# Kernel tuning notes

Hardware: AMD Instinct MI355X
Metric: run time of the kernel (lower is better)

Reference implementation:

```python
import jax, jax.numpy as jnp
import numpy as np

N0, N1, N2 = 1500, 6000, 4000
F_IN, F_OUT = 32, 32
K00, K0P = 2, 2
K1N, K11, K12, K1P = 2, 2, 2, 2
K2N, K22 = 2, 2


def chebyshev(L, k, x):
    # Chebyshev recursion: T1 = L x, T2 = 2 L T1 - x, T_j = 2 L T_{j-1} - T_{j-2}
    # Returns (n, F, k) stack of T1..Tk (identity term handled by caller).
    t_prev = L @ x
    terms = [t_prev]
    t_pp = x
    for _ in range(k - 1):
        t = 2.0 * (L @ t_prev) - t_pp
        t_pp, t_prev = t_prev, t
        terms.append(t)
    return jnp.stack(terms, axis=2)


def _sym(key, n):
    a = jax.random.normal(key, (n, n), jnp.float32) / jnp.sqrt(jnp.float32(n))
    return 0.5 * (a + a.T)


def setup_inputs():
    key = jax.random.key(0)
    ks = jax.random.split(key, 16)
    x0 = jax.random.normal(ks[0], (N0, F_IN), jnp.float32)
    x1 = jax.random.normal(ks[1], (N1, F_IN), jnp.float32)
    x2 = jax.random.normal(ks[2], (N2, F_IN), jnp.float32)
    B1 = jax.random.normal(ks[3], (N0, N1), jnp.float32) / jnp.sqrt(jnp.float32(N1))
    B2 = jax.random.normal(ks[4], (N1, N2), jnp.float32) / jnp.sqrt(jnp.float32(N2))
    L0 = _sym(ks[5], N0)
    L1l = _sym(ks[6], N1)
    L1u = _sym(ks[7], N1)
    L2 = _sym(ks[8], N2)
    # Degree matrices: diagonal with strictly positive entries (as in real SC data).
    D1 = jnp.diag(jax.random.uniform(ks[9], (N0,), jnp.float32, 0.5, 2.0))
    D2 = jnp.diag(jax.random.uniform(ks[10], (N1,), jnp.float32, 0.5, 2.0))
    D3 = jnp.diag(jax.random.uniform(ks[11], (N2,), jnp.float32, 0.5, 2.0))
    D5 = jnp.diag(jax.random.uniform(ks[12], (N1,), jnp.float32, 0.5, 2.0))
    W0 = jax.random.normal(ks[13], (F_IN, F_OUT, 1 + K00 + 1 + K0P), jnp.float32) * 0.05
    W1 = jax.random.normal(ks[14], (F_IN, F_OUT, 1 + K1N + 1 + K11 + K12 + 1 + K1P), jnp.float32) * 0.05
    W2 = jax.random.normal(ks[15], (F_IN, F_OUT, 1 + K2N + 1 + K22), jnp.float32) * 0.05
    return dict(x0=x0, x1=x1, x2=x2, B1=B1, B2=B2, L0=L0, L1l=L1l, L1u=L1u,
                L2=L2, D1=D1, D2=D2, D3=D3, D5=D5, W0=W0, W1=W1, W2=W2)


def _forward(x0, x1, x2, B1, B2, L0, L1l, L1u, L2, d1_inv, d2, d3, d5_pinv, W0, W1, W2):
    # ---- order 0 ----
    x0p = d1_inv[:, None] * (B1 @ x1)               # inv(D1) @ B1 @ x1
    X0 = jnp.concatenate([x0[:, :, None], chebyshev(L0, K00, x0),
                          x0p[:, :, None], chebyshev(L0, K0P, x0p)], axis=2)
    # ---- order 1 ----
    x1n = d2[:, None] * (B1.T @ (d1_inv[:, None] * x0))  # D2 @ B1.T @ inv(D1) @ x0
    x1p = B2 @ (d3[:, None] * x2)                        # B2 @ D3 @ x2
    X1 = jnp.concatenate([x1n[:, :, None], chebyshev(L1l, K1N, x1n),
                          x1[:, :, None], chebyshev(L1l, K11, x1), chebyshev(L1u, K12, x1),
                          x1p[:, :, None], chebyshev(L1u, K1P, x1p)], axis=2)
    # ---- order 2 ----
    x2n = B2.T @ (d5_pinv[:, None] * x1)                 # B2.T @ pinv(D5) @ x1
    X2 = jnp.concatenate([x2n[:, :, None], chebyshev(L2, K2N, x2n),
                          x2[:, :, None], chebyshev(L2, K22, x2)], axis=2)
    y0 = jax.nn.relu(jnp.einsum('nik,iok->no', X0, W0))
    y1 = jax.nn.relu(jnp.einsum('nik,iok->no', X1, W1))
    y2 = jax.nn.relu(jnp.einsum('nik,iok->no', X2, W2))
    return (y0, y1, y2)


def reference(x0, x1, x2, B1, B2, L0, L1l, L1u, L2, D1, D2, D3, D5, W0, W1, W2):
    # D matrices are diagonal degree matrices; inverse/pinverse of a diagonal
    # matrix is the diagonal of (safe) reciprocals -- identical math to
    # torch.inverse / torch.pinverse on these inputs, without an O(n^3) solve.
    d1_inv = 1.0 / jnp.diag(D1)
    d2 = jnp.diag(D2)
    d3 = jnp.diag(D3)
    d5 = jnp.diag(D5)
    d5_pinv = jnp.where(d5 != 0, 1.0 / d5, 0.0)
    return _forward(x0, x1, x2, B1, B2, L0, L1l, L1u, L2, d1_inv, d2, d3, d5_pinv, W0, W1, W2)
```

## Files before the change

kernel.cpp:

```cpp
#include <hip/hip_runtime.h>
#include <stdint.h>

typedef __attribute__((ext_vector_type(4))) float f32x4;
typedef __attribute__((ext_vector_type(8))) short s16x8;
typedef unsigned short us;

static __device__ __forceinline__ us f2bf(float f) {
  union { float f; uint32_t u; } v; v.f = f;
  uint32_t u = v.u;
  u += 0x7fffu + ((u >> 16) & 1u);
  return (us)(u >> 16);
}

static __device__ __forceinline__ float dval(const float* dv, long r, long dstr, int mode) {
  if (!dv || mode == 0) return 1.f;
  float d = dv[r * dstr];
  if (mode == 2) return (d != 0.f) ? 1.f / d : 0.f;
  return d;
}

static __device__ void tpose_tile(const float* __restrict__ src, long lds_, int n,
                                  const float* __restrict__ dv, long dstr, int mode,
                                  us* __restrict__ dst, int ldn, int tile,
                                  us (*sm)[72]) {
  const int t = threadIdx.x;
  const int r0 = tile * 64;
  {
    const int rr = t & 63;
    const int cg = t >> 6;
    const int gr = r0 + rr;
    float sc = 1.f;
    f32x4 v0 = {0.f, 0.f, 0.f, 0.f}, v1 = {0.f, 0.f, 0.f, 0.f};
    if (gr < n) {
      sc = dval(dv, gr, dstr, mode);
      const float* sp = src + (long)gr * lds_ + cg * 8;
      v0 = *(const f32x4*)sp;
      v1 = *(const f32x4*)(sp + 4);
    }
#pragma unroll
    for (int j = 0; j < 4; ++j) {
      sm[cg * 8 + j][rr] = f2bf(v0[j] * sc);
      sm[cg * 8 + 4 + j][rr] = f2bf(v1[j] * sc);
    }
  }
  __syncthreads();
  {
    const int f = t >> 3;
    const int nc = (t & 7) * 8;
    if (r0 + nc < ldn) {
      s16x8 v = *(const s16x8*)&sm[f][nc];
      *(s16x8*)(dst + (size_t)f * ldn + r0 + nc) = v;
    }
  }
}

struct TSeg { const float* src; us* dst; long lds_; int n, ldn, start; };
struct TPack { TSeg t[8]; int nseg; };

__global__ __launch_bounds__(256) void tpose_batch(TPack P) {
  __shared__ us sm[32][72];
  int b = blockIdx.x;
  int si = P.nseg - 1;
  while (si > 0 && P.t[si].start > b) --si;
  const TSeg s = P.t[si];
  tpose_tile(s.src, s.lds_, s.n, nullptr, 0, 0, s.dst, s.ldn, b - s.start, sm);
}

__global__ __launch_bounds__(256) void prep(
    const float* __restrict__ x0, const float* __restrict__ x1, const float* __restrict__ x2,
    const float* __restrict__ D1, const float* __restrict__ D3, const float* __restrict__ D5,
    const float* __restrict__ W0, const float* __restrict__ W1, const float* __restrict__ W2,
    us* x0T, us* x0dT, us* x1T, us* x1dT, us* x2T, us* x2dT,
    us* W0T, us* W1T, us* W2T,
    float* __restrict__ X0a, float* __restrict__ X1a, float* __restrict__ X2a) {
  __shared__ us sm[32][72];
  int b = blockIdx.x;
  if (b < 24)  { tpose_tile(x0, 32, 1500, nullptr, 0, 0, x0T, 1536, b, sm); return; }
  b -= 24;
  if (b < 24)  { tpose_tile(x0, 32, 1500, D1, 1501, 2, x0dT, 1536, b, sm); return; }
  b -= 24;
  if (b < 94)  { tpose_tile(x1, 32, 6000, nullptr, 0, 0, x1T, 6016, b, sm); return; }
  b -= 94;
  if (b < 94)  { tpose_tile(x1, 32, 6000, D5, 6001, 2, x1dT, 6016, b, sm); return; }
  b -= 94;
  if (b < 63)  { tpose_tile(x2, 32, 4000, nullptr, 0, 0, x2T, 4032, b, sm); return; }
  b -= 63;
  if (b < 63)  { tpose_tile(x2, 32, 4000, D3, 4001, 1, x2dT, 4032, b, sm); return; }
  b -= 63;
  if (b < 3) {
    const float* W = (b == 0) ? W0 : ((b == 1) ? W1 : W2);
    us* dst = (b == 0) ? W0T : ((b == 1) ? W1T : W2T);
    const int K = (b == 1) ? 11 : 6;
    const int C = K * 32;
    const int CP = (b == 1) ? 384 : 192;
    for (int idx = threadIdx.x; idx < 32 * CP; idx += 256) {
      int o = idx / CP, j = idx - o * CP;
      float v = 0.f;
      if (j < C) { int k = j >> 5, i = j & 31; v = W[((long)i * 32 + o) * K + k]; }
      dst[(size_t)o * CP + j] = f2bf(v);
    }
    return;
  }
  b -= 3;
  const long V0 = 1500L * 48, V1 = 6000L * 88, V2 = 4000L * 48;
  for (long i = (long)b * 256 + threadIdx.x; i < V0 + V1 + V2; i += 512L * 256) {
    f32x4 v = {0.f, 0.f, 0.f, 0.f};
    float* dst;
    if (i < V0) {
      long r = i / 48; int c0 = (int)(i - r * 48) * 4;
      if (c0 < 32) v = *(const f32x4*)(x0 + r * 32 + c0);
      dst = X0a + r * 192 + c0;
    } else if (i < V0 + V1) {
      long j = i - V0; long r = j / 88; int c0 = (int)(j - r * 88) * 4;
      if (c0 >= 96 && c0 < 128) v = *(const f32x4*)(x1 + r * 32 + (c0 - 96));
      dst = X1a + r * 352 + c0;
    } else {
      long j = i - V0 - V1; long r = j / 48; int c0 = (int)(j - r * 48) * 4;
      if (c0 >= 96 && c0 < 128) v = *(const f32x4*)(x2 + r * 32 + (c0 - 96));
      dst = X2a + r * 192 + c0;
    }
    *(f32x4*)dst = v;
  }
}

struct CSeg { const float* in; us* out; int ldi, nI, nC, ldoT, cx, start; };
struct CPack { CSeg c[2]; int nseg; };

static __device__ void convT_tile(const float* __restrict__ in, int ldi, int nI, int nC,
                                  us* __restrict__ outT, int ldoT, int bx, int by,
                                  us (*sT)[72]) {
  const int t = threadIdx.x;
  const int tc0 = bx * 64;
  const int tr0 = by * 64;
  const int c0 = (t & 15) * 4;
  const int r0 = (t >> 4) * 4;
  us ub[4][4];
#pragma unroll
  for (int j = 0; j < 4; ++j) {
    int gr = tr0 + r0 + j;
    f32x4 v = {0.f, 0.f, 0.f, 0.f};
    if (gr < nI) {
      const float* pI = in + (size_t)gr * ldi + tc0 + c0;
      if (tc0 + c0 + 3 < nC) {
        v = *(const f32x4*)pI;
      } else {
#pragma unroll
        for (int jj = 0; jj < 4; ++jj) if (tc0 + c0 + jj < nC) v[jj] = pI[jj];
      }
    }
#pragma unroll
    for (int jj = 0; jj < 4; ++jj) ub[j][jj] = f2bf(v[jj]);
  }
#pragma unroll
  for (int jj = 0; jj < 4; ++jj) {
    union { us u[4]; unsigned long long ll; } w;
#pragma unroll
    for (int j = 0; j < 4; ++j) w.u[j] = ub[j][jj];
    *(unsigned long long*)&sT[c0 + jj][r0] = w.ll;
  }
  __syncthreads();
#pragma unroll
  for (int p = 0; p < 2; ++p) {
    int orow = (t >> 3) + p * 32;
    int rcol = (t & 7) * 8;
    int grow = tc0 + orow;
    int gcol = tr0 + rcol;
    if (grow < nC && gcol < ldoT) {
      union { unsigned long long ll[2]; s16x8 v; } w;
      w.ll[0] = *(const unsigned long long*)&sT[orow][rcol];
      w.ll[1] = *(const unsigned long long*)&sT[orow][rcol + 4];
      *(s16x8*)(outT + (size_t)grow * ldoT + gcol) = w.v;
    }
  }
}

__global__ __launch_bounds__(256) void convT_batch(CPack P) {
  __shared__ us sT[64][72];
  int b = blockIdx.x;
  int si = P.nseg - 1;
  while (si > 0 && P.c[si].start > b) --si;
  const CSeg s = P.c[si];
  int local = b - s.start;
  convT_tile(s.in, s.ldi, s.nI, s.nC, s.out, s.ldoT, local % s.cx, local / s.cx, sT);
}

struct Seg {
  const void* A; const us* Bt0; const us* Bt1;
  const float* S0; const float* S1; const float* sv;
  float* C0; float* C1;
  long lda, ldS, sstr, ldc;
  float alpha, beta;
  int n_rows, n_k, ldb, smode, kchunk, tiles, ky, start;
};
struct SegPack { Seg s[4]; int nseg; };

template <int F, bool RELU, typename AT>
__global__ __launch_bounds__(256) void mm_batch(SegPack P) {
  __shared__ __align__(16) us sA[64 * 64];
  __shared__ __align__(16) us sX[64 * 64];

  int b = blockIdx.x;
  int si = P.nseg - 1;
  while (si > 0 && P.s[si].start > b) --si;
  const Seg sg = P.s[si];
  const int local = b - sg.start;
  const int bx = local % sg.tiles;
  const int kidx = local / sg.tiles;

  const AT* __restrict__ A = (const AT*)sg.A;
  const int n_rows = sg.n_rows, n_k = sg.n_k, ldb = sg.ldb;
  const long lda = sg.lda;

  const int tid = threadIdx.x;
  const int k_begin = kidx * sg.kchunk;
  const int k_end = min(n_k, k_begin + sg.kchunk);
  const int nsteps = (k_end - k_begin + 63) >> 6;

  const int srow = tid >> 2;
  const int sslot = tid & 3;
  const int kc_off = sslot * 16;
  const long arowg = (long)bx * 64 + srow;
  const bool arow_ok = arowg < n_rows;
  const bool xrow_ok = (F == 64) || (srow < 32);
  const us* xbase = ((srow < 32) ? sg.Bt0 : sg.Bt1) + (size_t)(srow & 31) * ldb;

  s16x8 abf0 = (s16x8)0, abf1 = (s16x8)0;
  f32x4 af0, af1, af2, af3;
  s16x8 x0r = (s16x8)0, x1r = (s16x8)0;

  auto load_tiles = [&](int k0) {
    int kc = k0 + kc_off;
    if constexpr (sizeof(AT) == 4) {
      af0 = f32x4{0, 0, 0, 0}; af1 = af0; af2 = af0; af3 = af0;
      if (arow_ok) {
        const float* ap = (const float*)A + (size_t)arowg * lda + kc;
        if (kc + 15 < n_k) {
          af0 = *(const f32x4*)ap; af1 = *(const f32x4*)(ap + 4);
          af2 = *(const f32x4*)(ap + 8); af3 = *(const f32x4*)(ap + 12);
        } else {
#pragma unroll
          for (int j = 0; j < 4; ++j) {
            if (kc + j < n_k) af0[j] = ap[j];
            if (kc + 4 + j < n_k) af1[j] = ap[4 + j];
            if (kc + 8 + j < n_k) af2[j] = ap[8 + j];
            if (kc + 12 + j < n_k) af3[j] = ap[12 + j];
          }
        }
      }
    } else {
      abf0 = (s16x8)0; abf1 = (s16x8)0;
      if (arow_ok) {
        const us* ap = (const us*)A + (size_t)arowg * lda + kc;
        if (kc + 15 < n_k) {
          abf0 = *(const s16x8*)ap; abf1 = *(const s16x8*)(ap + 8);
        } else {
#pragma unroll
          for (int j = 0; j < 8; ++j) {
            if (kc + j < n_k) abf0[j] = (short)ap[j];
            if (kc + 8 + j < n_k) abf1[j] = (short)ap[8 + j];
          }
        }
      }
    }
    if (xrow_ok) {
      x0r = *(const s16x8*)(xbase + kc);
      x1r = *(const s16x8*)(xbase + kc + 8);
    }
  };

  load_tiles(k_begin);

  const int wave = tid >> 6;
  const int lane = tid & 63;
  const int g = lane >> 4;
  const int r = lane & 15;
  const int wslot0 = ((2 * sslot) ^ (srow & 7)) * 8;
  const int wslot1 = ((2 * sslot + 1) ^ (srow & 7)) * 8;

  f32x4 acc[F / 16];
#pragma unroll
  for (int i = 0; i < F / 16; ++i) acc[i] = f32x4{0.f, 0.f, 0.f, 0.f};

  for (int s = 0; s < nsteps; ++s) {
    s16x8 pk0, pk1;
    if constexpr (sizeof(AT) == 4) {
#pragma unroll
      for (int j = 0; j < 4; ++j) {
        pk0[j] = (short)f2bf(af0[j]); pk0[4 + j] = (short)f2bf(af1[j]);
        pk1[j] = (short)f2bf(af2[j]); pk1[4 + j] = (short)f2bf(af3[j]);
      }
    } else { pk0 = abf0; pk1 = abf1; }
    *(s16x8*)&sA[srow * 64 + wslot0] = pk0;
    *(s16x8*)&sA[srow * 64 + wslot1] = pk1;
    if (xrow_ok) {
      *(s16x8*)&sX[srow * 64 + wslot0] = x0r;
      *(s16x8*)&sX[srow * 64 + wslot1] = x1r;
    }
    __syncthreads();
    if (s + 1 < nsteps) load_tiles(k_begin + (s + 1) * 64);

    const int arow = wave * 16 + r;
#pragma unroll
    for (int kk = 0; kk < 2; ++kk) {
      s16x8 afr = *(s16x8*)&sA[arow * 64 + (((kk * 4 + g) ^ (arow & 7)) << 3)];
#pragma unroll
      for (int nt = 0; nt < F / 16; ++nt) {
        int xc = nt * 16 + r;
        s16x8 bfr = *(s16x8*)&sX[xc * 64 + (((kk * 4 + g) ^ (xc & 7)) << 3)];
        acc[nt] = __builtin_amdgcn_mfma_f32_16x16x32_bf16(afr, bfr, acc[nt], 0, 0, 0);
      }
    }
    __syncthreads();
  }

  float svv[4];
#pragma unroll
  for (int j = 0; j < 4; ++j) {
    long row = (long)bx * 64 + wave * 16 + g * 4 + j;
    svv[j] = (row < n_rows) ? dval(sg.sv, row, sg.sstr, sg.smode) : 0.f;
  }
#pragma unroll
  for (int nt = 0; nt < F / 16; ++nt) {
    float* C = (F == 64 && nt >= 2) ? sg.C1 : sg.C0;
    const float* S = (F == 64 && nt >= 2) ? sg.S1 : sg.S0;
    int col = ((F == 64) ? (nt & 1) : nt) * 16 + r;
#pragma unroll
    for (int j = 0; j < 4; ++j) {
      long row = (long)bx * 64 + wave * 16 + g * 4 + j;
      if (row < n_rows) {
        float v = sg.alpha * acc[nt][j] * svv[j];
        if (S && (sg.ky == 1 || kidx == 0)) v += sg.beta * S[row * sg.ldS + col];
        if (sg.ky > 1) {
          atomicAdd(&C[row * sg.ldc + col], v);
        } else {
          if (RELU) v = fmaxf(v, 0.0f);
          C[row * sg.ldc + col] = v;
        }
      }
    }
  }
}

__global__ void colcopy(float* __restrict__ dst, const float* __restrict__ src, int n,
                        const float* __restrict__ dv, long dstr, int mode) {
  int idx = blockIdx.x * 256 + threadIdx.x;
  if (idx >= n * 32) return;
  dst[idx] = src[idx] * dval(dv, idx >> 5, dstr, mode);
}
__global__ void scale_ld(float* __restrict__ dst, long ld, int n,
                         const float* __restrict__ dv, long dstr, int mode) {
  int idx = blockIdx.x * 256 + threadIdx.x;
  if (idx >= n * 32) return;
  dst[(size_t)(idx >> 5) * ld + (idx & 31)] *= dval(dv, idx >> 5, dstr, mode);
}
__global__ __launch_bounds__(256) void mm_at(
    const float* __restrict__ A, int lda, int m,
    const float* __restrict__ X,
    float* __restrict__ C, int ldc, int n, int kchunk) {
  const int fg = threadIdx.x & 3;
  const int cg = threadIdx.x >> 2;
  const int c = blockIdx.x * 256 + cg * 4;
  const int k0 = blockIdx.y * kchunk;
  const int k1 = min(m, k0 + kchunk);
  const int f = fg * 8;
  float acc[4][8];
#pragma unroll
  for (int a = 0; a < 4; ++a)
#pragma unroll
    for (int b = 0; b < 8; ++b) acc[a][b] = 0.f;
  for (int k = k0; k < k1; ++k) {
    const float* Ar = A + (size_t)k * lda + c;
    f32x4 a;
    if (c + 3 < n) a = *(const f32x4*)Ar;
    else {
      a = f32x4{0.f, 0.f, 0.f, 0.f};
#pragma unroll
      for (int j = 0; j < 4; ++j) if (c + j < n) a[j] = Ar[j];
    }
    f32x4 xa = *(const f32x4*)(X + (size_t)k * 32 + f);
    f32x4 xb = *(const f32x4*)(X + (size_t)k * 32 + f + 4);
#pragma unroll
    for (int cc = 0; cc < 4; ++cc)
#pragma unroll
      for (int jj = 0; jj < 4; ++jj) {
        acc[cc][jj] += a[cc] * xa[jj];
        acc[cc][4 + jj] += a[cc] * xb[jj];
      }
  }
  if (c >= n) return;
#pragma unroll
  for (int cc = 0; cc < 4; ++cc) {
    if (c + cc >= n) break;
#pragma unroll
    for (int jj = 0; jj < 8; ++jj)
      atomicAdd(&C[(size_t)(c + cc) * ldc + f + jj], acc[cc][jj]);
  }
}


extern "C" void kernel_launch(void* const* d_in, const int* in_sizes, int n_in,
                              void* d_out, int out_size, void* d_ws, size_t ws_size,
                              hipStream_t stream) {
  (void)in_sizes; (void)n_in; (void)out_size;
  const float* x0  = (const float*)d_in[0];
  const float* x1  = (const float*)d_in[1];
  const float* x2  = (const float*)d_in[2];
  const float* B1  = (const float*)d_in[3];
  const float* B2  = (const float*)d_in[4];
  const float* L0  = (const float*)d_in[5];
  const float* L1l = (const float*)d_in[6];
  const float* L1u = (const float*)d_in[7];
  const float* L2  = (const float*)d_in[8];
  const float* D1  = (const float*)d_in[9];
  const float* D2  = (const float*)d_in[10];
  const float* D3  = (const float*)d_in[11];
  const float* D5  = (const float*)d_in[12];
  const float* W0  = (const float*)d_in[13];
  const float* W1  = (const float*)d_in[14];
  const float* W2  = (const float*)d_in[15];
  float* out = (float*)d_out;

  char* p = (char*)d_ws;
  auto alloc = [&](size_t b) { char* r = p; p += (b + 255) & ~(size_t)255; return r; };

  us* x0T   = (us*)alloc((size_t)32 * 1536 * 2);
  us* x0dT  = (us*)alloc((size_t)32 * 1536 * 2);
  us* x1T   = (us*)alloc((size_t)32 * 6016 * 2);
  us* x1dT  = (us*)alloc((size_t)32 * 6016 * 2);
  us* x2T   = (us*)alloc((size_t)32 * 4032 * 2);
  us* x2dT  = (us*)alloc((size_t)32 * 4032 * 2);
  us* x0pT  = (us*)alloc((size_t)32 * 1536 * 2);
  us* x1nT  = (us*)alloc((size_t)32 * 6016 * 2);
  us* x1pT  = (us*)alloc((size_t)32 * 6016 * 2);
  us* x2nT  = (us*)alloc((size_t)32 * 4032 * 2);
  us* T1a0T = (us*)alloc((size_t)32 * 1536 * 2);
  us* T1b0T = (us*)alloc((size_t)32 * 1536 * 2);
  us* T1laT = (us*)alloc((size_t)32 * 6016 * 2);
  us* T1lbT = (us*)alloc((size_t)32 * 6016 * 2);
  us* T1uaT = (us*)alloc((size_t)32 * 6016 * 2);
  us* T1ubT = (us*)alloc((size_t)32 * 6016 * 2);
  us* T1a2T = (us*)alloc((size_t)32 * 4032 * 2);
  us* T1b2T = (us*)alloc((size_t)32 * 4032 * 2);
  us* W0T   = (us*)alloc((size_t)32 * 192 * 2);
  us* W1T   = (us*)alloc((size_t)32 * 384 * 2);
  us* W2T   = (us*)alloc((size_t)32 * 192 * 2);

  float* X0a = (float*)alloc((size_t)1500 * 192 * 4);
  float* X1a = (float*)alloc((size_t)6000 * 352 * 4);
  float* X2a = (float*)alloc((size_t)4000 * 192 * 4);

  float* z0  = (float*)alloc((size_t)1500 * 32 * 4);
  float* sx1 = (float*)alloc((size_t)6000 * 32 * 4);

  size_t used = (size_t)(p - (char*)d_ws);
  bool haveT = used + (size_t)6000 * 1536 * 2 + (size_t)4000 * 6016 * 2 <= ws_size;
  us* B1t = nullptr; us* B2t = nullptr;
  if (haveT) {
    B1t = (us*)alloc((size_t)6000 * 1536 * 2);
    B2t = (us*)alloc((size_t)4000 * 6016 * 2);
  }

  auto nb = [](long t) { return (unsigned)((t + 255) / 256); };

  auto seg = [](const void* A, long lda, int n_rows, int n_k,
                const us* Bt0, const us* Bt1, int ldb,
                float alpha, const float* S0, const float* S1, long ldS, float beta,
                const float* sv, long sstr, int smode,
                float* C0, float* C1, long ldc,
                int kchunk, int tiles, int ky, int start) {
    Seg s;
    s.A = A; s.Bt0 = Bt0; s.Bt1 = Bt1; s.S0 = S0; s.S1 = S1; s.sv = sv;
    s.C0 = C0; s.C1 = C1; s.lda = lda; s.ldS = ldS; s.sstr = sstr; s.ldc = ldc;
    s.alpha = alpha; s.beta = beta; s.n_rows = n_rows; s.n_k = n_k; s.ldb = ldb;
    s.smode = smode; s.kchunk = kchunk; s.tiles = tiles; s.ky = ky; s.start = start;
    return s;
  };

  prep<<<877, 256, 0, stream>>>(x0, x1, x2, D1, D3, D5, W0, W1, W2,
                                x0T, x0dT, x1T, x1dT, x2T, x2dT, W0T, W1T, W2T,
                                X0a, X1a, X2a);

  {
    SegPack P{};
    P.nseg = 2;
    P.s[0] = seg(B1, 6000, 1500, 6000, x1T, x1T, 6016,
                 1.f, nullptr, nullptr, 0, 0.f, D1, 1501, 2,
                 X0a + 3 * 32, nullptr, 192, 768, 24, 8, 0);
    P.s[1] = seg(B2, 4000, 6000, 4000, x2dT, x2dT, 4032,
                 1.f, nullptr, nullptr, 0, 0.f, nullptr, 0, 0,
                 X1a + 8 * 32, nullptr, 352, 1344, 94, 3, 192);
    mm_batch<32, false, float><<<474, 256, 0, stream>>>(P);
  }

  if (haveT) {
    CPack P{};
    P.nseg = 2;
    P.c[0] = CSeg{B1, B1t, 6000, 1500, 6000, 1536, 94, 0};
    P.c[1] = CSeg{B2, B2t, 4000, 6000, 4000, 6016, 63, 2256};
    convT_batch<<<8178, 256, 0, stream>>>(P);
  }

  if (haveT) {
    SegPack P{};
    P.nseg = 2;
    P.s[0] = seg(B1t, 1536, 6000, 1536, x0dT, x0dT, 1536,
                 1.f, nullptr, nullptr, 0, 0.f, D2, 6001, 1,
                 X1a + 0 * 32, nullptr, 352, 768, 94, 2, 0);
    P.s[1] = seg(B2t, 6016, 4000, 6016, x1dT, x1dT, 6016,
                 1.f, nullptr, nullptr, 0, 0.f, nullptr, 0, 0,
                 X2a + 0 * 32, nullptr, 192, 1536, 63, 4, 188);
    mm_batch<32, false, us><<<440, 256, 0, stream>>>(P);
  } else {
    colcopy<<<nb(1500L * 32), 256, 0, stream>>>(z0, x0, 1500, D1, 1501, 2);
    mm_at<<<dim3(24, 24), 256, 0, stream>>>(B1, 6000, 1500, z0, X1a + 0 * 32, 352, 6000, 63);
    scale_ld<<<nb(6000L * 32), 256, 0, stream>>>(X1a + 0 * 32, 352, 6000, D2, 6001, 1);
    colcopy<<<nb(6000L * 32), 256, 0, stream>>>(sx1, x1, 6000, D5, 6001, 2);
    mm_at<<<dim3(16, 32), 256, 0, stream>>>(B2, 4000, 6000, sx1, X2a + 0 * 32, 192, 4000, 188);
  }

  {
    TPack P{};
    P.nseg = 4;
    P.t[0] = TSeg{X0a + 3 * 32, x0pT, 192, 1500, 1536, 0};
    P.t[1] = TSeg{X1a + 0 * 32, x1nT, 352, 6000, 6016, 24};
    P.t[2] = TSeg{X1a + 8 * 32, x1pT, 352, 6000, 6016, 118};
    P.t[3] = TSeg{X2a + 0 * 32, x2nT, 192, 4000, 4032, 212};
    tpose_batch<<<275, 256, 0, stream>>>(P);
  }

  {
    SegPack P{};
    P.nseg = 4;
    P.s[0] = seg(L0, 1500, 1500, 1500, x0T, x0pT, 1536,
                 1.f, nullptr, nullptr, 0, 0.f, nullptr, 0, 0,
                 X0a + 1 * 32, X0a + 4 * 32, 192, 768, 24, 2, 0);
    P.s[1] = seg(L1l, 6000, 6000, 6000, x1nT, x1T, 6016,
                 1.f, nullptr, nullptr, 0, 0.f, nullptr, 0, 0,
                 X1a + 1 * 32, X1a + 4 * 32, 352, 3008, 94, 2, 48);
    P.s[2] = seg(L1u, 6000, 6000, 6000, x1T, x1pT, 6016,
                 1.f, nullptr, nullptr, 0, 0.f, nullptr, 0, 0,
                 X1a + 6 * 32, X1a + 9 * 32, 352, 3008, 94, 2, 236);
    P.s[3] = seg(L2, 4000, 4000, 4000, x2nT, x2T, 4032,
                 1.f, nullptr, nullptr, 0, 0.f, nullptr, 0, 0,
                 X2a + 1 * 32, X2a + 4 * 32, 192, 2048, 63, 2, 424);
    mm_batch<64, false, float><<<550, 256, 0, stream>>>(P);
  }

  {
    TPack P{};
    P.nseg = 8;
    P.t[0] = TSeg{X0a + 1 * 32, T1a0T, 192, 1500, 1536, 0};
    P.t[1] = TSeg{X0a + 4 * 32, T1b0T, 192, 1500, 1536, 24};
    P.t[2] = TSeg{X1a + 1 * 32, T1laT, 352, 6000, 6016, 48};
    P.t[3] = TSeg{X1a + 4 * 32, T1lbT, 352, 6000, 6016, 142};
    P.t[4] = TSeg{X1a + 6 * 32, T1uaT, 352, 6000, 6016, 236};
    P.t[5] = TSeg{X1a + 9 * 32, T1ubT, 352, 6000, 6016, 330};
    P.t[6] = TSeg{X2a + 1 * 32, T1a2T, 192, 4000, 4032, 424};
    P.t[7] = TSeg{X2a + 4 * 32, T1b2T, 192, 4000, 4032, 487};
    tpose_batch<<<550, 256, 0, stream>>>(P);
  }

  {
    SegPack P{};
    P.nseg = 4;
    P.s[0] = seg(L0, 1500, 1500, 1500, T1a0T, T1b0T, 1536,
                 2.f, X0a + 0 * 32, X0a + 3 * 32, 192, -1.f, nullptr, 0, 0,
                 X0a + 2 * 32, X0a + 5 * 32, 192, 768, 24, 2, 0);
    P.s[1] = seg(L1l, 6000, 6000, 6000, T1laT, T1lbT, 6016,
                 2.f, X1a + 0 * 32, X1a + 3 * 32, 352, -1.f, nullptr, 0, 0,
                 X1a + 2 * 32, X1a + 5 * 32, 352, 3008, 94, 2, 48);
    P.s[2] = seg(L1u, 6000, 6000, 6000, T1uaT, T1ubT, 6016,
                 2.f, X1a + 3 * 32, X1a + 8 * 32, 352, -1.f, nullptr, 0, 0,
                 X1a + 7 * 32, X1a + 10 * 32, 352, 3008, 94, 2, 236);
    P.s[3] = seg(L2, 4000, 4000, 4000, T1a2T, T1b2T, 4032,
                 2.f, X2a + 0 * 32, X2a + 3 * 32, 192, -1.f, nullptr, 0, 0,
                 X2a + 2 * 32, X2a + 5 * 32, 192, 2048, 63, 2, 424);
    mm_batch<64, false, float><<<550, 256, 0, stream>>>(P);
  }

  {
    SegPack P{};
    P.nseg = 3;
    P.s[0] = seg(X0a, 192, 1500, 192, W0T, W0T, 192,
                 1.f, nullptr, nullptr, 0, 0.f, nullptr, 0, 0,
                 out, nullptr, 32, 192, 24, 1, 0);
    P.s[1] = seg(X1a, 352, 6000, 352, W1T, W1T, 384,
                 1.f, nullptr, nullptr, 0, 0.f, nullptr, 0, 0,
                 out + 48000, nullptr, 32, 384, 94, 1, 24);
    P.s[2] = seg(X2a, 192, 4000, 192, W2T, W2T, 192,
                 1.f, nullptr, nullptr, 0, 0.f, nullptr, 0, 0,
                 out + 240000, nullptr, 32, 192, 118, 1, 118);
    mm_batch<32, true, float><<<181, 256, 0, stream>>>(P);
  }
}
```

Before: 319.1 us.

## Cache bf16 Laplacians on first pass and fuse conversion/transposes into GEMM launches

The first Chebyshev GEMM now writes the bf16-converted Laplacian rows it already computes into workspace buffers, so the second Chebyshev GEMM reads half-size bf16 operands instead of fp32. The B1/B2 transpose-convert blocks are merged into the first GEMM launch, and two of the transposes are merged into the B-transposed GEMM, which cuts launches and lets independent work overlap. The change adds extra bf16 write traffic in the first pass and depends on the workspace being large enough, with fallback tiers when it is not. The last GEMM's tile count for the order-2 segment changes from 118 to 63.

```diff
diff --git a/kernel.cpp b/kernel.cpp
--- a/kernel.cpp
+++ b/kernel.cpp
@@ -54,7 +54,55 @@
   }
 }
 
-struct TSeg { const float* src; us* dst; long lds_; int n, ldn, start; };
+static __device__ void convT_tile(const float* __restrict__ in, int ldi, int nI, int nC,
+                                  us* __restrict__ outT, int ldoT, int bx, int by,
+                                  us (*sT)[72]) {
+  const int t = threadIdx.x;
+  const int tc0 = bx * 64;
+  const int tr0 = by * 64;
+  const int c0 = (t & 15) * 4;
+  const int r0 = (t >> 4) * 4;
+  us ub[4][4];
+#pragma unroll
+  for (int j = 0; j < 4; ++j) {
+    int gr = tr0 + r0 + j;
+    f32x4 v = {0.f, 0.f, 0.f, 0.f};
+    if (gr < nI) {
+      const float* pI = in + (size_t)gr * ldi + tc0 + c0;
+      if (tc0 + c0 + 3 < nC) {
+        v = *(const f32x4*)pI;
+      } else {
+#pragma unroll
+        for (int jj = 0; jj < 4; ++jj) if (tc0 + c0 + jj < nC) v[jj] = pI[jj];
+      }
+    }
+#pragma unroll
+    for (int jj = 0; jj < 4; ++jj) ub[j][jj] = f2bf(v[jj]);
+  }
+#pragma unroll
+  for (int jj = 0; jj < 4; ++jj) {
+    union { us u[4]; unsigned long long ll; } w;
+#pragma unroll
+    for (int j = 0; j < 4; ++j) w.u[j] = ub[j][jj];
+    *(unsigned long long*)&sT[c0 + jj][r0] = w.ll;
+  }
+  __syncthreads();
+#pragma unroll
+  for (int p = 0; p < 2; ++p) {
+    int orow = (t >> 3) + p * 32;
+    int rcol = (t & 7) * 8;
+    int grow = tc0 + orow;
+    int gcol = tr0 + rcol;
+    if (grow < nC && gcol < ldoT) {
+      union { unsigned long long ll[2]; s16x8 v; } w;
+      w.ll[0] = *(const unsigned long long*)&sT[orow][rcol];
+      w.ll[1] = *(const unsigned long long*)&sT[orow][rcol + 4];
+      *(s16x8*)(outT + (size_t)grow * ldoT + gcol) = w.v;
+    }
+  }
+}
+
+struct TSeg { const float* src; us* dst; int lds_, n, ldn, start; };
 struct TPack { TSeg t[8]; int nseg; };
 
 __global__ __launch_bounds__(256) void tpose_batch(TPack P) {
@@ -123,83 +171,46 @@
   }
 }
 
-struct CSeg { const float* in; us* out; int ldi, nI, nC, ldoT, cx, start; };
-struct CPack { CSeg c[2]; int nseg; };
-
-static __device__ void convT_tile(const float* __restrict__ in, int ldi, int nI, int nC,
-                                  us* __restrict__ outT, int ldoT, int bx, int by,
-                                  us (*sT)[72]) {
-  const int t = threadIdx.x;
-  const int tc0 = bx * 64;
-  const int tr0 = by * 64;
-  const int c0 = (t & 15) * 4;
-  const int r0 = (t >> 4) * 4;
-  us ub[4][4];
-#pragma unroll
-  for (int j = 0; j < 4; ++j) {
-    int gr = tr0 + r0 + j;
-    f32x4 v = {0.f, 0.f, 0.f, 0.f};
-    if (gr < nI) {
-      const float* pI = in + (size_t)gr * ldi + tc0 + c0;
-      if (tc0 + c0 + 3 < nC) {
-        v = *(const f32x4*)pI;
-      } else {
-#pragma unroll
-        for (int jj = 0; jj < 4; ++jj) if (tc0 + c0 + jj < nC) v[jj] = pI[jj];
-      }
-    }
-#pragma unroll
-    for (int jj = 0; jj < 4; ++jj) ub[j][jj] = f2bf(v[jj]);
-  }
-#pragma unroll
-  for (int jj = 0; jj < 4; ++jj) {
-    union { us u[4]; unsigned long long ll; } w;
-#pragma unroll
-    for (int j = 0; j < 4; ++j) w.u[j] = ub[j][jj];
-    *(unsigned long long*)&sT[c0 + jj][r0] = w.ll;
-  }
-  __syncthreads();
-#pragma unroll
-  for (int p = 0; p < 2; ++p) {
-    int orow = (t >> 3) + p * 32;
-    int rcol = (t & 7) * 8;
-    int grow = tc0 + orow;
-    int gcol = tr0 + rcol;
-    if (grow < nC && gcol < ldoT) {
-      union { unsigned long long ll[2]; s16x8 v; } w;
-      w.ll[0] = *(const unsigned long long*)&sT[orow][rcol];
-      w.ll[1] = *(const unsigned long long*)&sT[orow][rcol + 4];
-      *(s16x8*)(outT + (size_t)grow * ldoT + gcol) = w.v;
-    }
-  }
-}
-
-__global__ __launch_bounds__(256) void convT_batch(CPack P) {
-  __shared__ us sT[64][72];
-  int b = blockIdx.x;
-  int si = P.nseg - 1;
-  while (si > 0 && P.c[si].start > b) --si;
-  const CSeg s = P.c[si];
-  int local = b - s.start;
-  convT_tile(s.in, s.ldi, s.nI, s.nC, s.out, s.ldoT, local % s.cx, local / s.cx, sT);
-}
-
 struct Seg {
-  const void* A; const us* Bt0; const us* Bt1;
+  const void* A; us* Aout;
+  const us* Bt0; const us* Bt1;
   const float* S0; const float* S1; const float* sv;
   float* C0; float* C1;
-  long lda, ldS, sstr, ldc;
   float alpha, beta;
+  int lda, ldao, ldS, sstr, ldc;
   int n_rows, n_k, ldb, smode, kchunk, tiles, ky, start;
 };
-struct SegPack { Seg s[4]; int nseg; };
+struct CSeg { const float* in; us* out; int ldi, nI, nC, ldoT, cx, start; };
+struct Mega {
+  Seg s[4]; CSeg c[2]; TSeg t[2];
+  int nseg, gemm_end, nconv, conv_end, ntp;
+};
 
 template <int F, bool RELU, typename AT>
-__global__ __launch_bounds__(256) void mm_batch(SegPack P) {
-  __shared__ __align__(16) us sA[64 * 64];
-  __shared__ __align__(16) us sX[64 * 64];
-
-  int b = blockIdx.x;
+__global__ __launch_bounds__(256) void mega(Mega P) {
+  __shared__ __align__(16) us lds[64 * 128];
+  const int b = blockIdx.x;
+  if (b >= P.gemm_end) {
+    if (b < P.conv_end) {
+      int lb = b - P.gemm_end;
+      int si = P.nconv - 1;
+      while (si > 0 && P.c[si].start > lb) --si;
+      const CSeg s = P.c[si];
+      int l = lb - s.start;
+      convT_tile(s.in, s.ldi, s.nI, s.nC, s.out, s.ldoT, l % s.cx, l / s.cx, (us(*)[72])lds);
+    } else {
+      int lb = b - P.conv_end;
+      int si = P.ntp - 1;
+      while (si > 0 && P.t[si].start > lb) --si;
+      const TSeg s = P.t[si];
+      tpose_tile(s.src, s.lds_, s.n, nullptr, 0, 0, s.dst, s.ldn, lb - s.start, (us(*)[72])lds);
+    }
+    return;
+  }
+
+  us* sA = lds;
+  us* sX = lds + 64 * 64;
+
   int si = P.nseg - 1;
   while (si > 0 && P.s[si].start > b) --si;
   const Seg sg = P.s[si];
@@ -209,7 +220,6 @@
 
   const AT* __restrict__ A = (const AT*)sg.A;
   const int n_rows = sg.n_rows, n_k = sg.n_k, ldb = sg.ldb;
-  const long lda = sg.lda;
 
   const int tid = threadIdx.x;
   const int k_begin = kidx * sg.kchunk;
@@ -233,7 +243,7 @@
     if constexpr (sizeof(AT) == 4) {
       af0 = f32x4{0, 0, 0, 0}; af1 = af0; af2 = af0; af3 = af0;
       if (arow_ok) {
-        const float* ap = (const float*)A + (size_t)arowg * lda + kc;
+        const float* ap = (const float*)A + (size_t)arowg * sg.lda + kc;
         if (kc + 15 < n_k) {
           af0 = *(const f32x4*)ap; af1 = *(const f32x4*)(ap + 4);
           af2 = *(const f32x4*)(ap + 8); af3 = *(const f32x4*)(ap + 12);
@@ -250,7 +260,7 @@
     } else {
       abf0 = (s16x8)0; abf1 = (s16x8)0;
       if (arow_ok) {
-        const us* ap = (const us*)A + (size_t)arowg * lda + kc;
+        const us* ap = (const us*)A + (size_t)arowg * sg.lda + kc;
         if (kc + 15 < n_k) {
           abf0 = *(const s16x8*)ap; abf1 = *(const s16x8*)(ap + 8);
         } else {
@@ -289,6 +299,11 @@
         pk0[j] = (short)f2bf(af0[j]); pk0[4 + j] = (short)f2bf(af1[j]);
         pk1[j] = (short)f2bf(af2[j]); pk1[4 + j] = (short)f2bf(af3[j]);
       }
+      if (sg.Aout && arow_ok) {
+        us* q = sg.Aout + (size_t)arowg * sg.ldao + (k_begin + s * 64 + kc_off);
+        *(s16x8*)q = pk0;
+        *(s16x8*)(q + 8) = pk1;
+      }
     } else { pk0 = abf0; pk1 = abf1; }
     *(s16x8*)&sA[srow * 64 + wslot0] = pk0;
     *(s16x8*)&sA[srow * 64 + wslot1] = pk1;
@@ -329,12 +344,12 @@
       long row = (long)bx * 64 + wave * 16 + g * 4 + j;
       if (row < n_rows) {
         float v = sg.alpha * acc[nt][j] * svv[j];
-        if (S && (sg.ky == 1 || kidx == 0)) v += sg.beta * S[row * sg.ldS + col];
+        if (S && (sg.ky == 1 || kidx == 0)) v += sg.beta * S[row * (size_t)sg.ldS + col];
         if (sg.ky > 1) {
-          atomicAdd(&C[row * sg.ldc + col], v);
+          atomicAdd(&C[row * (size_t)sg.ldc + col], v);
         } else {
           if (RELU) v = fmaxf(v, 0.0f);
-          C[row * sg.ldc + col] = v;
+          C[row * (size_t)sg.ldc + col] = v;
         }
       }
     }
@@ -453,26 +468,43 @@
   float* sx1 = (float*)alloc((size_t)6000 * 32 * 4);
 
   size_t used = (size_t)(p - (char*)d_ws);
-  bool haveT = used + (size_t)6000 * 1536 * 2 + (size_t)4000 * 6016 * 2 <= ws_size;
-  us* B1t = nullptr; us* B2t = nullptr;
-  if (haveT) {
+  const size_t needB  = (size_t)6000 * 1536 * 2 + (size_t)4000 * 6016 * 2 + 1024;
+  const size_t needL1 = 2 * (size_t)6000 * 6016 * 2 + 1024;
+  const size_t needL02 = (size_t)1500 * 1536 * 2 + (size_t)4000 * 4032 * 2 + 1024;
+  bool haveB = used + needB <= ws_size;
+  int tier = 0;
+  if (haveB) {
+    if (used + needB + needL1 + needL02 <= ws_size) tier = 2;
+    else if (used + needB + needL1 <= ws_size) tier = 1;
+  }
+  us *B1t = nullptr, *B2t = nullptr;
+  us *L0bf = nullptr, *L1lbf = nullptr, *L1ubf = nullptr, *L2bf = nullptr;
+  if (haveB) {
     B1t = (us*)alloc((size_t)6000 * 1536 * 2);
     B2t = (us*)alloc((size_t)4000 * 6016 * 2);
   }
+  if (tier >= 1) {
+    L1lbf = (us*)alloc((size_t)6000 * 6016 * 2);
+    L1ubf = (us*)alloc((size_t)6000 * 6016 * 2);
+  }
+  if (tier >= 2) {
+    L0bf = (us*)alloc((size_t)1500 * 1536 * 2);
+    L2bf = (us*)alloc((size_t)4000 * 4032 * 2);
+  }
 
   auto nb = [](long t) { return (unsigned)((t + 255) / 256); };
-
-  auto seg = [](const void* A, long lda, int n_rows, int n_k,
+  auto seg = [](const void* A, us* Aout, int lda, int ldao, int n_rows, int n_k,
                 const us* Bt0, const us* Bt1, int ldb,
-                float alpha, const float* S0, const float* S1, long ldS, float beta,
-                const float* sv, long sstr, int smode,
-                float* C0, float* C1, long ldc,
+                float alpha, const float* S0, const float* S1, int ldS, float beta,
+                const float* sv, int sstr, int smode,
+                float* C0, float* C1, int ldc,
                 int kchunk, int tiles, int ky, int start) {
     Seg s;
-    s.A = A; s.Bt0 = Bt0; s.Bt1 = Bt1; s.S0 = S0; s.S1 = S1; s.sv = sv;
-    s.C0 = C0; s.C1 = C1; s.lda = lda; s.ldS = ldS; s.sstr = sstr; s.ldc = ldc;
-    s.alpha = alpha; s.beta = beta; s.n_rows = n_rows; s.n_k = n_k; s.ldb = ldb;
-    s.smode = smode; s.kchunk = kchunk; s.tiles = tiles; s.ky = ky; s.start = start;
+    s.A = A; s.Aout = Aout; s.Bt0 = Bt0; s.Bt1 = Bt1; s.S0 = S0; s.S1 = S1; s.sv = sv;
+    s.C0 = C0; s.C1 = C1; s.alpha = alpha; s.beta = beta;
+    s.lda = lda; s.ldao = ldao; s.ldS = ldS; s.sstr = sstr; s.ldc = ldc;
+    s.n_rows = n_rows; s.n_k = n_k; s.ldb = ldb; s.smode = smode;
+    s.kchunk = kchunk; s.tiles = tiles; s.ky = ky; s.start = start;
     return s;
   };
 
@@ -481,115 +513,168 @@
                                 X0a, X1a, X2a);
 
   {
-    SegPack P{};
+    Mega P{};
     P.nseg = 2;
-    P.s[0] = seg(B1, 6000, 1500, 6000, x1T, x1T, 6016,
+    P.s[0] = seg(B1, nullptr, 6000, 0, 1500, 6000, x1T, x1T, 6016,
                  1.f, nullptr, nullptr, 0, 0.f, D1, 1501, 2,
                  X0a + 3 * 32, nullptr, 192, 768, 24, 8, 0);
-    P.s[1] = seg(B2, 4000, 6000, 4000, x2dT, x2dT, 4032,
+    P.s[1] = seg(B2, nullptr, 4000, 0, 6000, 4000, x2dT, x2dT, 4032,
                  1.f, nullptr, nullptr, 0, 0.f, nullptr, 0, 0,
                  X1a + 8 * 32, nullptr, 352, 1344, 94, 3, 192);
-    mm_batch<32, false, float><<<474, 256, 0, stream>>>(P);
-  }
-
-  if (haveT) {
-    CPack P{};
+    P.gemm_end = 474;
+    if (haveB) {
+      P.nconv = 2;
+      P.c[0] = CSeg{B1, B1t, 6000, 1500, 6000, 1536, 94, 0};
+      P.c[1] = CSeg{B2, B2t, 4000, 6000, 4000, 6016, 63, 2256};
+      P.conv_end = 474 + 8178;
+    } else {
+      P.nconv = 0; P.conv_end = 474;
+    }
+    P.ntp = 0;
+    mega<32, false, float><<<P.conv_end, 256, 0, stream>>>(P);
+  }
+
+  if (haveB) {
+    Mega P{};
     P.nseg = 2;
-    P.c[0] = CSeg{B1, B1t, 6000, 1500, 6000, 1536, 94, 0};
-    P.c[1] = CSeg{B2, B2t, 4000, 6000, 4000, 6016, 63, 2256};
-    convT_batch<<<8178, 256, 0, stream>>>(P);
-  }
-
-  if (haveT) {
-    SegPack P{};
-    P.nseg = 2;
-    P.s[0] = seg(B1t, 1536, 6000, 1536, x0dT, x0dT, 1536,
+    P.s[0] = seg(B1t, nullptr, 1536, 0, 6000, 1536, x0dT, x0dT, 1536,
                  1.f, nullptr, nullptr, 0, 0.f, D2, 6001, 1,
                  X1a + 0 * 32, nullptr, 352, 768, 94, 2, 0);
-    P.s[1] = seg(B2t, 6016, 4000, 6016, x1dT, x1dT, 6016,
+    P.s[1] = seg(B2t, nullptr, 6016, 0, 4000, 6016, x1dT, x1dT, 6016,
                  1.f, nullptr, nullptr, 0, 0.f, nullptr, 0, 0,
                  X2a + 0 * 32, nullptr, 192, 1536, 63, 4, 188);
-    mm_batch<32, false, us><<<440, 256, 0, stream>>>(P);
+    P.gemm_end = 440;
+    P.nconv = 0; P.conv_end = 440;
+    P.ntp = 2;
+    P.t[0] = TSeg{X0a + 3 * 32, x0pT, 192, 1500, 1536, 0};
+    P.t[1] = TSeg{X1a + 8 * 32, x1pT, 352, 6000, 6016, 24};
+    mega<32, false, us><<<558, 256, 0, stream>>>(P);
   } else {
     colcopy<<<nb(1500L * 32), 256, 0, stream>>>(z0, x0, 1500, D1, 1501, 2);
     mm_at<<<dim3(24, 24), 256, 0, stream>>>(B1, 6000, 1500, z0, X1a + 0 * 32, 352, 6000, 63);
     scale_ld<<<nb(6000L * 32), 256, 0, stream>>>(X1a + 0 * 32, 352, 6000, D2, 6001, 1);
     colcopy<<<nb(6000L * 32), 256, 0, stream>>>(sx1, x1, 6000, D5, 6001, 2);
     mm_at<<<dim3(16, 32), 256, 0, stream>>>(B2, 4000, 6000, sx1, X2a + 0 * 32, 192, 4000, 188);
-  }
-
-  {
-    TPack P{};
+    TPack T{};
+    T.nseg = 2;
+    T.t[0] = TSeg{X0a + 3 * 32, x0pT, 192, 1500, 1536, 0};
+    T.t[1] = TSeg{X1a + 8 * 32, x1pT, 352, 6000, 6016, 24};
+    tpose_batch<<<118, 256, 0, stream>>>(T);
+  }
+
+  {
+    TPack T{};
+    T.nseg = 2;
+    T.t[0] = TSeg{X1a + 0 * 32, x1nT, 352, 6000, 6016, 0};
+    T.t[1] = TSeg{X2a + 0 * 32, x2nT, 192, 4000, 4032, 94};
+    tpose_batch<<<157, 256, 0, stream>>>(T);
+  }
+
+  {
+    Mega P{};
     P.nseg = 4;
-    P.t[0] = TSeg{X0a + 3 * 32, x0pT, 192, 1500, 1536, 0};
-    P.t[1] = TSeg{X1a + 0 * 32, x1nT, 352, 6000, 6016, 24};
-    P.t[2] = TSeg{X1a + 8 * 32, x1pT, 352, 6000, 6016, 118};
-    P.t[3] = TSeg{X2a + 0 * 32, x2nT, 192, 4000, 4032, 212};
-    tpose_batch<<<275, 256, 0, stream>>>(P);
-  }
-
-  {
-    SegPack P{};
-    P.nseg = 4;
-    P.s[0] = seg(L0, 1500, 1500, 1500, x0T, x0pT, 1536,
+    P.s[0] = seg(L0, L0bf, 1500, 1536, 1500, 1500, x0T, x0pT, 1536,
                  1.f, nullptr, nullptr, 0, 0.f, nullptr, 0, 0,
                  X0a + 1 * 32, X0a + 4 * 32, 192, 768, 24, 2, 0);
-    P.s[1] = seg(L1l, 6000, 6000, 6000, x1nT, x1T, 6016,
+    P.s[1] = seg(L1l, L1lbf, 6000, 6016, 6000, 6000, x1nT, x1T, 6016,
                  1.f, nullptr, nullptr, 0, 0.f, nullptr, 0, 0,
                  X1a + 1 * 32, X1a + 4 * 32, 352, 3008, 94, 2, 48);
-    P.s[2] = seg(L1u, 6000, 6000, 6000, x1T, x1pT, 6016,
+    P.s[2] = seg(L1u, L1ubf, 6000, 6016, 6000, 6000, x1T, x1pT, 6016,
                  1.f, nullptr, nullptr, 0, 0.f, nullptr, 0, 0,
                  X1a + 6 * 32, X1a + 9 * 32, 352, 3008, 94, 2, 236);
-    P.s[3] = seg(L2, 4000, 4000, 4000, x2nT, x2T, 4032,
+    P.s[3] = seg(L2, L2bf, 4000, 4032, 4000, 4000, x2nT, x2T, 4032,
                  1.f, nullptr, nullptr, 0, 0.f, nullptr, 0, 0,
                  X2a + 1 * 32, X2a + 4 * 32, 192, 2048, 63, 2, 424);
-    mm_batch<64, false, float><<<550, 256, 0, stream>>>(P);
-  }
-
-  {
-    TPack P{};
-    P.nseg = 8;
-    P.t[0] = TSeg{X0a + 1 * 32, T1a0T, 192, 1500, 1536, 0};
-    P.t[1] = TSeg{X0a + 4 * 32, T1b0T, 192, 1500, 1536, 24};
-    P.t[2] = TSeg{X1a + 1 * 32, T1laT, 352, 6000, 6016, 48};
-    P.t[3] = TSeg{X1a + 4 * 32, T1lbT, 352, 6000, 6016, 142};
-    P.t[4] = TSeg{X1a + 6 * 32, T1uaT, 352, 6000, 6016, 236};
-    P.t[5] = TSeg{X1a + 9 * 32, T1ubT, 352, 6000, 6016, 330};
-    P.t[6] = TSeg{X2a + 1 * 32, T1a2T, 192, 4000, 4032, 424};
-    P.t[7] = TSeg{X2a + 4 * 32, T1b2T, 192, 4000, 4032, 487};
-    tpose_batch<<<550, 256, 0, stream>>>(P);
-  }
-
-  {
-    SegPack P{};
-    P.nseg = 4;
-    P.s[0] = seg(L0, 1500, 1500, 1500, T1a0T, T1b0T, 1536,
-                 2.f, X0a + 0 * 32, X0a + 3 * 32, 192, -1.f, nullptr, 0, 0,
-                 X0a + 2 * 32, X0a + 5 * 32, 192, 768, 24, 2, 0);
-    P.s[1] = seg(L1l, 6000, 6000, 6000, T1laT, T1lbT, 6016,
-                 2.f, X1a + 0 * 32, X1a + 3 * 32, 352, -1.f, nullptr, 0, 0,
-                 X1a + 2 * 32, X1a + 5 * 32, 352, 3008, 94, 2, 48);
-    P.s[2] = seg(L1u, 6000, 6000, 6000, T1uaT, T1ubT, 6016,
-                 2.f, X1a + 3 * 32, X1a + 8 * 32, 352, -1.f, nullptr, 0, 0,
-                 X1a + 7 * 32, X1a + 10 * 32, 352, 3008, 94, 2, 236);
-    P.s[3] = seg(L2, 4000, 4000, 4000, T1a2T, T1b2T, 4032,
-                 2.f, X2a + 0 * 32, X2a + 3 * 32, 192, -1.f, nullptr, 0, 0,
-                 X2a + 2 * 32, X2a + 5 * 32, 192, 2048, 63, 2, 424);
-    mm_batch<64, false, float><<<550, 256, 0, stream>>>(P);
-  }
-
-  {
-    SegPack P{};
+    P.gemm_end = 550; P.nconv = 0; P.conv_end = 550; P.ntp = 0;
+    mega<64, false, float><<<550, 256, 0, stream>>>(P);
+  }
+
+  {
+    TPack T{};
+    T.nseg = 8;
+    T.t[0] = TSeg{X0a + 1 * 32, T1a0T, 192, 1500, 1536, 0};
+    T.t[1] = TSeg{X0a + 4 * 32, T1b0T, 192, 1500, 1536, 24};
+    T.t[2] = TSeg{X1a + 1 * 32, T1laT, 352, 6000, 6016, 48};
+    T.t[3] = TSeg{X1a + 4 * 32, T1lbT, 352, 6000, 6016, 142};
+    T.t[4] = TSeg{X1a + 6 * 32, T1uaT, 352, 6000, 6016, 236};
+    T.t[5] = TSeg{X1a + 9 * 32, T1ubT, 352, 6000, 6016, 330};
+    T.t[6] = TSeg{X2a + 1 * 32, T1a2T, 192, 4000, 4032, 424};
+    T.t[7] = TSeg{X2a + 4 * 32, T1b2T, 192, 4000, 4032, 487};
+    tpose_batch<<<550, 256, 0, stream>>>(T);
+  }
+
+  {
+    if (tier == 2) {
+      Mega P{};
+      P.nseg = 4;
+      P.s[0] = seg(L0bf, nullptr, 1536, 0, 1500, 1536, T1a0T, T1b0T, 1536,
+                   2.f, X0a + 0 * 32, X0a + 3 * 32, 192, -1.f, nullptr, 0, 0,
+                   X0a + 2 * 32, X0a + 5 * 32, 192, 768, 24, 2, 0);
+      P.s[1] = seg(L1lbf, nullptr, 6016, 0, 6000, 6016, T1laT, T1lbT, 6016,
+                   2.f, X1a + 0 * 32, X1a + 3 * 32, 352, -1.f, nullptr, 0, 0,
+                   X1a + 2 * 32, X1a + 5 * 32, 352, 3008, 94, 2, 48);
+      P.s[2] = seg(L1ubf, nullptr, 6016, 0, 6000, 6016, T1uaT, T1ubT, 6016,
+                   2.f, X1a + 3 * 32, X1a + 8 * 32, 352, -1.f, nullptr, 0, 0,
+                   X1a + 7 * 32, X1a + 10 * 32, 352, 3008, 94, 2, 236);
+      P.s[3] = seg(L2bf, nullptr, 4032, 0, 4000, 4032, T1a2T, T1b2T, 4032,
+                   2.f, X2a + 0 * 32, X2a + 3 * 32, 192, -1.f, nullptr, 0, 0,
+                   X2a + 2 * 32, X2a + 5 * 32, 192, 2048, 63, 2, 424);
+      P.gemm_end = 550; P.nconv = 0; P.conv_end = 550; P.ntp = 0;
+      mega<64, false, us><<<550, 256, 0, stream>>>(P);
+    } else if (tier == 1) {
+      Mega P{};
+      P.nseg = 2;
+      P.s[0] = seg(L1lbf, nullptr, 6016, 0, 6000, 6016, T1laT, T1lbT, 6016,
+                   2.f, X1a + 0 * 32, X1a + 3 * 32, 352, -1.f, nullptr, 0, 0,
+                   X1a + 2 * 32, X1a + 5 * 32, 352, 3008, 94, 2, 0);
+      P.s[1] = seg(L1ubf, nullptr, 6016, 0, 6000, 6016, T1uaT, T1ubT, 6016,
+                   2.f, X1a + 3 * 32, X1a + 8 * 32, 352, -1.f, nullptr, 0, 0,
+                   X1a + 7 * 32, X1a + 10 * 32, 352, 3008, 94, 2, 188);
+      P.gemm_end = 376; P.nconv = 0; P.conv_end = 376; P.ntp = 0;
+      mega<64, false, us><<<376, 256, 0, stream>>>(P);
+      Mega Q{};
+      Q.nseg = 2;
+      Q.s[0] = seg(L0, nullptr, 1500, 0, 1500, 1500, T1a0T, T1b0T, 1536,
+                   2.f, X0a + 0 * 32, X0a + 3 * 32, 192, -1.f, nullptr, 0, 0,
+                   X0a + 2 * 32, X0a + 5 * 32, 192, 768, 24, 2, 0);
+      Q.s[1] = seg(L2, nullptr, 4000, 0, 4000, 4000, T1a2T, T1b2T, 4032,
+                   2.f, X2a + 0 * 32, X2a + 3 * 32, 192, -1.f, nullptr, 0, 0,
+                   X2a + 2 * 32, X2a + 5 * 32, 192, 2048, 63, 2, 48);
+      Q.gemm_end = 174; Q.nconv = 0; Q.conv_end = 174; Q.ntp = 0;
+      mega<64, false, float><<<174, 256, 0, stream>>>(Q);
+    } else {
+      Mega P{};
+      P.nseg = 4;
+      P.s[0] = seg(L0, nullptr, 1500, 0, 1500, 1500, T1a0T, T1b0T, 1536,
+                   2.f, X0a + 0 * 32, X0a + 3 * 32, 192, -1.f, nullptr, 0, 0,
+                   X0a + 2 * 32, X0a + 5 * 32, 192, 768, 24, 2, 0);
+      P.s[1] = seg(L1l, nullptr, 6000, 0, 6000, 6000, T1laT, T1lbT, 6016,
+                   2.f, X1a + 0 * 32, X1a + 3 * 32, 352, -1.f, nullptr, 0, 0,
+                   X1a + 2 * 32, X1a + 5 * 32, 352, 3008, 94, 2, 48);
+      P.s[2] = seg(L1u, nullptr, 6000, 0, 6000, 6000, T1uaT, T1ubT, 6016,
+                   2.f, X1a + 3 * 32, X1a + 8 * 32, 352, -1.f, nullptr, 0, 0,
+                   X1a + 7 * 32, X1a + 10 * 32, 352, 3008, 94, 2, 236);
+      P.s[3] = seg(L2, nullptr, 4000, 0, 4000, 4000, T1a2T, T1b2T, 4032,
+                   2.f, X2a + 0 * 32, X2a + 3 * 32, 192, -1.f, nullptr, 0, 0,
+                   X2a + 2 * 32, X2a + 5 * 32, 192, 2048, 63, 2, 424);
+      P.gemm_end = 550; P.nconv = 0; P.conv_end = 550; P.ntp = 0;
+      mega<64, false, float><<<550, 256, 0, stream>>>(P);
+    }
+  }
+
+  {
+    Mega P{};
     P.nseg = 3;
-    P.s[0] = seg(X0a, 192, 1500, 192, W0T, W0T, 192,
+    P.s[0] = seg(X0a, nullptr, 192, 0, 1500, 192, W0T, W0T, 192,
                  1.f, nullptr, nullptr, 0, 0.f, nullptr, 0, 0,
                  out, nullptr, 32, 192, 24, 1, 0);
-    P.s[1] = seg(X1a, 352, 6000, 352, W1T, W1T, 384,
+    P.s[1] = seg(X1a, nullptr, 352, 0, 6000, 352, W1T, W1T, 384,
                  1.f, nullptr, nullptr, 0, 0.f, nullptr, 0, 0,
                  out + 48000, nullptr, 32, 384, 94, 1, 24);
-    P.s[2] = seg(X2a, 192, 4000, 192, W2T, W2T, 192,
-                 1.f, nullptr, nullptr, 0, 0.f, nullptr, 0, 0,
-                 out + 240000, nullptr, 32, 192, 118, 1, 118);
-    mm_batch<32, true, float><<<181, 256, 0, stream>>>(P);
-  }
-}
+    P.s[2] = seg(X2a, nullptr, 192, 0, 4000, 192, W2T, W2T, 192,
+                 1.f, nullptr, nullptr, 0, 0.f, nullptr, 0, 0,
+                 out + 240000, nullptr, 32, 192, 63, 1, 118);
+    P.gemm_end = 181; P.nconv = 0; P.conv_end = 181; P.ntp = 0;
+    mega<32, true, float><<<181, 256, 0, stream>>>(P);
+  }
+}
```

Result: faster. 309.3 us (-3.1%).
